# Kernel tuning notes

Hardware: AMD Instinct MI355X
Metric: run time of the kernel (lower is better)

## Reference

```python
import jax, jax.numpy as jnp
import numpy as np

B, N, DIM, H = 8, 1024, 512, 8
D = DIM // H
SCALE = DIM ** -0.5


def setup_inputs() -> dict:
    key = jax.random.key(0)
    ks = jax.random.split(key, 8)
    s = 0.02
    return {
        "x": jax.random.normal(ks[0], (B, N, DIM), dtype=jnp.float32),
        "mask": jax.random.uniform(ks[1], (1, 1, N, N), dtype=jnp.float32),
        "Wqkv1": jax.random.normal(ks[2], (DIM, 3 * DIM), dtype=jnp.float32) * s,
        "bqkv1": jnp.zeros((3 * DIM,), dtype=jnp.float32),
        "Wqkv2": jax.random.normal(ks[3], (DIM, 3 * DIM), dtype=jnp.float32) * s,
        "bqkv2": jnp.zeros((3 * DIM,), dtype=jnp.float32),
        "Wnn1": jax.random.normal(ks[4], (DIM, DIM), dtype=jnp.float32) * s,
        "bnn1": jnp.zeros((DIM,), dtype=jnp.float32),
    }


def _split_heads(qkv, b, n):
    # qkv: [b, n, 3*dim] -> three [b, h, n, d]
    q, k, v = jnp.split(qkv, 3, axis=-1)
    r = lambda t: t.reshape(b, n, H, D).transpose(0, 2, 1, 3)
    return r(q), r(k), r(v)


def reference(x, mask, Wqkv1, bqkv1, Wqkv2, bqkv2, Wnn1, bnn1):
    b, n, dim = x.shape
    # Stage 1: mask-scaled sigmoid attention (no softmax, no scale)
    q, k, v = _split_heads(x @ Wqkv1 + bqkv1, b, n)
    dots = jax.nn.sigmoid(jnp.einsum('bhid,bhjd->bhij', q, k) * mask)
    out1 = jnp.einsum('bhij,bhjd->bhid', dots, v)
    out1 = out1.transpose(0, 2, 1, 3).reshape(b, n, dim)
    # Stage 2: standard scaled softmax attention on stage-1 output
    q, k, v = _split_heads(out1 @ Wqkv2 + bqkv2, b, n)
    attn = jax.nn.softmax(jnp.einsum('bhid,bhjd->bhij', q, k) * SCALE, axis=-1)
    out = jnp.einsum('bhij,bhjd->bhid', attn, v)
    out = out.transpose(0, 2, 1, 3).reshape(b, n, dim)
    # Output projection (dropout is identity in eval mode)
    return out @ Wnn1 + bnn1
```

## Files before the change

### kernel.cpp

```cpp
#include <hip/hip_runtime.h>
#include <hip/hip_bf16.h>
#include <stdint.h>

constexpr int B_ = 8, N_ = 1024, DIM_ = 512, H_ = 8, D_ = 64;
constexpr int BH_ = B_ * H_;
constexpr int M_  = B_ * N_;
constexpr float SCALE_ = 0.04419417382415922f;
constexpr float LOG2E_ = 1.44269504088896f;
constexpr float QSL2E_ = SCALE_ * LOG2E_;

typedef __bf16 bf16x8 __attribute__((ext_vector_type(8)));
typedef float  f32x4  __attribute__((ext_vector_type(4)));
typedef unsigned short u16;
typedef u16 u16x8 __attribute__((ext_vector_type(8)));
typedef u16 u16x4 __attribute__((ext_vector_type(4)));

static __device__ __forceinline__ u16 f2bf(float f) {
  return __builtin_bit_cast(u16, (__bf16)f);
}
static __device__ __forceinline__ bf16x8 ld8(const u16* p) {
  return __builtin_bit_cast(bf16x8, *reinterpret_cast<const u16x8*>(p));
}
static __device__ __forceinline__ f32x4 mfma16(bf16x8 a, bf16x8 b, f32x4 c) {
  return __builtin_amdgcn_mfma_f32_16x16x32_bf16(a, b, c, 0, 0, 0);
}
static __device__ __forceinline__ void gload_lds16(const u16* g, void* l) {
  __builtin_amdgcn_global_load_lds(
      (const __attribute__((address_space(1))) void*)g,
      (__attribute__((address_space(3))) void*)l, 16, 0, 0);
}
#define LGKM0() asm volatile("s_waitcnt lgkmcnt(0)" ::: "memory")
#define VMW(n)  asm volatile("s_waitcnt vmcnt(" #n ")" ::: "memory")

__global__ void k_prep(const float* __restrict__ x, const float* __restrict__ mask,
                       const float* __restrict__ W1, const float* __restrict__ W2,
                       const float* __restrict__ W3,
                       u16* __restrict__ xb, float* __restrict__ mk,
                       u16* __restrict__ W1t, u16* __restrict__ W2t, u16* __restrict__ W3t)
{
  const int b = blockIdx.x, t = threadIdx.x;
  if (b < 4096) {
    int idx = b * 256 + t;
    float4 v = reinterpret_cast<const float4*>(x)[idx];
    u16x4 o; o[0] = f2bf(v.x); o[1] = f2bf(v.y); o[2] = f2bf(v.z); o[3] = f2bf(v.w);
    reinterpret_cast<u16x4*>(xb)[idx] = o;
  } else if (b < 5120) {
    int idx = (b - 4096) * 256 + t;
    float4 v = reinterpret_cast<const float4*>(mask)[idx];
    v.x *= -LOG2E_; v.y *= -LOG2E_; v.z *= -LOG2E_; v.w *= -LOG2E_;
    reinterpret_cast<float4*>(mk)[idx] = v;
  } else if (b < 8192) {
    int idx = (b - 5120) * 256 + t;
    int c = idx >> 9, k = idx & 511;
    W1t[idx] = f2bf(W1[k * 1536 + c]);
  } else if (b < 11264) {
    int idx = (b - 8192) * 256 + t;
    int c = idx >> 9, k = idx & 511;
    float v = W2[k * 1536 + c];
    if (c < 512) v *= QSL2E_;
    W2t[idx] = f2bf(v);
  } else {
    int idx = (b - 11264) * 256 + t;
    int c = idx >> 9, k = idx & 511;
    W3t[idx] = f2bf(W3[k * 512 + c]);
  }
}

template<int NC, int MODE, bool SQ>
__global__ __launch_bounds__(256) void k_gemm(
    const u16* __restrict__ A, const u16* __restrict__ Wt, const float* __restrict__ bias,
    u16* __restrict__ qo, u16* __restrict__ ko, u16* __restrict__ vto, float* __restrict__ fo)
{
  __shared__ __attribute__((aligned(16))) u16 As[2][128 * 32];
  __shared__ __attribute__((aligned(16))) u16 Bs[2][128 * 32];
  const int wv = threadIdx.x >> 6, ln = threadIdx.x & 63;
  const int lr = ln & 15, lg = ln >> 4;
  const int wr = wv >> 1, wc = wv & 1;
  const int nwg = gridDim.x * gridDim.y;
  const int lin = blockIdx.y * gridDim.x + blockIdx.x;
  const int swz = (lin & 7) * (nwg >> 3) + (lin >> 3);
  const int r0 = (swz & 63) * 128;
  const int c0 = (swz >> 6) * 128;

  auto stage = [&](int bufi, int kk) {
#pragma unroll
    for (int q = 0; q < 2; ++q) {
      int L = (wv * 2 + q) * 1024 + ln * 16;
      int row = L >> 6;
      int col = ((L & 63) ^ (((row >> 1) & 3) << 4)) >> 1;
      gload_lds16(A  + (size_t)(r0 + row) * 512 + kk + col, (char*)As[bufi] + (wv * 2 + q) * 1024);
      gload_lds16(Wt + (size_t)(c0 + row) * 512 + kk + col, (char*)Bs[bufi] + (wv * 2 + q) * 1024);
    }
  };
  auto swzld = [&](const u16* tile, int row, int colb) -> bf16x8 {
    int byte = (row << 6) + (colb ^ (((row >> 1) & 3) << 4));
    return __builtin_bit_cast(bf16x8, *reinterpret_cast<const u16x8*>((const char*)tile + byte));
  };

  f32x4 acc[4][4] = {};
  stage(0, 0);
  int buf = 0;
  for (int kk = 0; kk < 512; kk += 32) {
    __syncthreads();
    if (kk + 32 < 512) stage(buf ^ 1, kk + 32);
    bf16x8 af[4], bfb[4];
#pragma unroll
    for (int m = 0; m < 4; ++m) af[m]  = swzld(As[buf], wr * 64 + m * 16 + lr, lg * 16);
#pragma unroll
    for (int n = 0; n < 4; ++n) bfb[n] = swzld(Bs[buf], wc * 64 + n * 16 + lr, lg * 16);
#pragma unroll
    for (int m = 0; m < 4; ++m)
#pragma unroll
      for (int n = 0; n < 4; ++n)
        acc[m][n] = mfma16(af[m], bfb[n], acc[m][n]);
    buf ^= 1;
  }

#pragma unroll
  for (int m = 0; m < 4; ++m)
#pragma unroll
    for (int n = 0; n < 4; ++n) {
      const int gc  = c0 + wc * 64 + n * 16 + lr;
      const int gr0 = r0 + wr * 64 + m * 16 + lg * 4;
      const float bsc = (SQ && gc < 512) ? QSL2E_ : 1.f;
      const float bv = bias[gc] * bsc;
      if (MODE == 0) {
        const int part = gc >> 9, cc = gc & 511;
        const int hh = cc >> 6, dd = cc & 63;
        const int bb = gr0 >> 10, nn = gr0 & 1023;
        const int bh = bb * H_ + hh;
        if (part == 2) {
          u16x4 w;
#pragma unroll
          for (int r = 0; r < 4; ++r) w[r] = f2bf(acc[m][n][r] + bv);
          *reinterpret_cast<u16x4*>(&vto[((size_t)(bh * D_ + dd)) * N_ + nn]) = w;
        } else {
          u16* dst = (part == 0 ? qo : ko) + ((size_t)(bh * N_ + nn)) * D_ + dd;
#pragma unroll
          for (int r = 0; r < 4; ++r) dst[(size_t)r * D_] = f2bf(acc[m][n][r] + bv);
        }
      } else {
#pragma unroll
        for (int r = 0; r < 4; ++r)
          fo[(size_t)(gr0 + r) * NC + gc] = acc[m][n][r] + bv;
      }
    }
}

template<int STAGE>
__global__ __launch_bounds__(512) void k_attn(
    const u16* __restrict__ Q, const u16* __restrict__ K, const u16* __restrict__ Vt,
    const float* __restrict__ mask, u16* __restrict__ O)
{
  __shared__ __attribute__((aligned(16))) u16 Kb[3][64 * 64];
  __shared__ __attribute__((aligned(16))) u16 Vb[3][64 * 64];
  __shared__ __attribute__((aligned(16))) u16 pbuf[8][16][40];
  const int wv = threadIdx.x >> 6, ln = threadIdx.x & 63;
  const int lr = ln & 15, lg = ln >> 4;
  const int lin = blockIdx.y * gridDim.x + blockIdx.x;
  const int swz = (lin & 7) * 64 + (lin >> 3);
  const int bh = swz >> 3;
  const int i0 = (swz & 7) * 128 + wv * 16;
  const size_t base = (size_t)bh * N_ * D_;

  auto stageKV = [&](int bufi, int jt2) {
    int L = wv * 1024 + ln * 16;
    int row = L >> 7;
    int col = ((L & 127) ^ ((row & 7) << 4)) >> 1;
    gload_lds16(K  + base + (size_t)(jt2 + row) * 64 + col,  (char*)Kb[bufi] + wv * 1024);
    gload_lds16(Vt + base + (size_t)row * 1024 + jt2 + col,  (char*)Vb[bufi] + wv * 1024);
  };
  auto swzld = [&](const u16* tile, int row, int colb) -> bf16x8 {
    int byte = (row << 7) + (colb ^ ((row & 7) << 4));
    return __builtin_bit_cast(bf16x8, *reinterpret_cast<const u16x8*>((const char*)tile + byte));
  };

  bf16x8 aq0 = ld8(Q + base + (size_t)(i0 + lr) * D_ + lg * 8);
  bf16x8 aq1 = ld8(Q + base + (size_t)(i0 + lr) * D_ + 32 + lg * 8);

  f32x4 acco[4] = {};
  float ssum_ln = 0.f;

  float4 mk[4];
  const float* mrow = mask + (size_t)(i0 + lr) * N_;
  auto loadmask = [&](int jt2) {
#pragma unroll
    for (int js = 0; js < 4; ++js)
      mk[js] = *reinterpret_cast<const float4*>(&mrow[jt2 + js * 16 + lg * 4]);
  };
  if (STAGE == 1) loadmask(0);

  stageKV(0, 0);
  stageKV(1, 64);
  constexpr int NT = 16;
  for (int t = 0; t < NT; ++t) {
    LGKM0();
    __builtin_amdgcn_s_barrier();
    if (t + 2 < NT) stageKV((t + 2) % 3, (t + 2) * 64);
    if (STAGE == 1) {
      if (t == 0)       VMW(4);
      else if (t == 1)  VMW(8);
      else if (t < 14)  VMW(12);
      else if (t == 14) VMW(10);
      else              VMW(8);
    } else {
      if (t < 14)       VMW(4);
      else if (t == 14) VMW(2);
      else              VMW(0);
    }
    const int cur = t % 3;
    const u16* Kt = Kb[cur];
    const u16* Vtl = Vb[cur];

    f32x4 s[4];
    __builtin_amdgcn_s_setprio(1);
#pragma unroll
    for (int js = 0; js < 4; ++js) {
      int krow = js * 16 + lr;
      bf16x8 bk0 = swzld(Kt, krow, lg * 16);
      bf16x8 bk1 = swzld(Kt, krow, 64 + lg * 16);
      f32x4 z = {};
      z = mfma16(bk0, aq0, z);
      z = mfma16(bk1, aq1, z);
      s[js] = z;
    }
    __builtin_amdgcn_s_setprio(0);

    float ps = 0.f;
#pragma unroll
    for (int h = 0; h < 2; ++h) {
#pragma unroll
      for (int js2 = 0; js2 < 2; ++js2) {
        const int js = h * 2 + js2;
        u16x4 w;
        if (STAGE == 1) {
#pragma unroll
          for (int r = 0; r < 4; ++r) {
            float mkr = (r == 0) ? mk[js].x : (r == 1) ? mk[js].y : (r == 2) ? mk[js].z : mk[js].w;
            float e = exp2f(s[js][r] * mkr);
            w[r] = f2bf(__builtin_amdgcn_rcpf(1.f + e));
          }
        } else {
#pragma unroll
          for (int r = 0; r < 4; ++r) {
            float p = exp2f(s[js][r]);
            ps += p;
            w[r] = f2bf(p);
          }
        }
        *reinterpret_cast<u16x4*>(&pbuf[wv][lr][js2 * 16 + lg * 4]) = w;
      }
      bf16x8 ap = ld8(&pbuf[wv][lr][lg * 8]);
      __builtin_amdgcn_s_setprio(1);
#pragma unroll
      for (int db = 0; db < 4; ++db) {
        bf16x8 bv = swzld(Vtl, db * 16 + lr, h * 64 + lg * 16);
        acco[db] = mfma16(ap, bv, acco[db]);
      }
      __builtin_amdgcn_s_setprio(0);
    }
    if (STAGE == 2) ssum_ln += ps;
    if (STAGE == 1 && t + 1 < NT) loadmask((t + 1) * 64);
  }

  float inv[4];
  if (STAGE == 2) {
    float st = ssum_ln;
    st += __shfl_xor(st, 16);
    st += __shfl_xor(st, 32);
#pragma unroll
    for (int r = 0; r < 4; ++r)
      inv[r] = __builtin_amdgcn_rcpf(__shfl(st, lg * 4 + r));
  }

  const int bb = bh >> 3, hh = bh & 7;
  u16* orow = O + (size_t)(bb * N_ + i0 + lr) * DIM_ + hh * D_;
#pragma unroll
  for (int h = 0; h < 2; ++h) {
#pragma unroll
    for (int db = 0; db < 2; ++db)
#pragma unroll
      for (int r = 0; r < 4; ++r) {
        float v = acco[h * 2 + db][r];
        if (STAGE == 2) v *= inv[r];
        pbuf[wv][lg * 4 + r][db * 16 + lr] = f2bf(v);
      }
    bf16x8 ov = ld8(&pbuf[wv][lr][lg * 8]);
    *reinterpret_cast<u16x8*>(orow + h * 32 + lg * 8) = __builtin_bit_cast(u16x8, ov);
  }
}

extern "C" void kernel_launch(void* const* d_in, const int* in_sizes, int n_in,
                              void* d_out, int out_size, void* d_ws, size_t ws_size,
                              hipStream_t stream)
{
  const float* x    = (const float*)d_in[0];
  const float* mask = (const float*)d_in[1];
  const float* W1   = (const float*)d_in[2];
  const float* b1   = (const float*)d_in[3];
  const float* W2   = (const float*)d_in[4];
  const float* b2   = (const float*)d_in[5];
  const float* W3   = (const float*)d_in[6];
  const float* b3   = (const float*)d_in[7];
  float* out = (float*)d_out;

  char* ws = (char*)d_ws;
  size_t off = 0;
  auto alloc = [&](size_t bytes) { char* p = ws + off; off += (bytes + 255) & ~255ULL; return p; };
  u16*   W1t = (u16*)alloc((size_t)1536 * 512 * 2);
  u16*   W2t = (u16*)alloc((size_t)1536 * 512 * 2);
  u16*   W3t = (u16*)alloc((size_t)512 * 512 * 2);
  u16*   xb  = (u16*)alloc((size_t)M_ * DIM_ * 2);
  u16*   q   = (u16*)alloc((size_t)BH_ * N_ * D_ * 2);
  u16*   k   = (u16*)alloc((size_t)BH_ * N_ * D_ * 2);
  u16*   vt  = (u16*)alloc((size_t)BH_ * N_ * D_ * 2);
  u16*   o1  = (u16*)alloc((size_t)M_ * DIM_ * 2);
  float* mk  = (float*)alloc((size_t)N_ * N_ * 4);
  u16*   o2  = xb;

  k_prep<<<12288, 256, 0, stream>>>(x, mask, W1, W2, W3, xb, mk, W1t, W2t, W3t);

  dim3 g1(M_ / 128, 1536 / 128);
  k_gemm<1536, 0, false><<<g1, 256, 0, stream>>>(xb, W1t, b1, q, k, vt, nullptr);

  dim3 ga(N_ / 128, BH_);
  k_attn<1><<<ga, 512, 0, stream>>>(q, k, vt, mk, o1);

  k_gemm<1536, 0, true><<<g1, 256, 0, stream>>>(o1, W2t, b2, q, k, vt, nullptr);

  k_attn<2><<<ga, 512, 0, stream>>>(q, k, vt, mk, o2);

  dim3 g3(M_ / 128, 512 / 128);
  k_gemm<512, 1, false><<<g3, 256, 0, stream>>>(o2, W3t, b3, nullptr, nullptr, nullptr, out);
}
```

Before: 227.1 us.

## Shrink attention blocks to 4 waves with double-buffered K/V and precomputed LDS offsets

The attention kernel now uses 256-thread blocks covering 64 query rows instead of 512-thread blocks covering 128, with a matching grid and block-index swizzle. The triple-buffered K/V ring with hand-tuned vmcnt waits becomes a double buffer guarded by __syncthreads, and the swizzled LDS read addresses are precomputed once. The aim is to raise occupancy and cut per-iteration address arithmetic. The cost is that K/V tiles are loaded twice as often across blocks, and the prefetch distance drops from two tiles to one.

```diff
diff --git a/kernel.cpp b/kernel.cpp
--- a/kernel.cpp
+++ b/kernel.cpp
@@ -21,6 +21,9 @@
 static __device__ __forceinline__ bf16x8 ld8(const u16* p) {
   return __builtin_bit_cast(bf16x8, *reinterpret_cast<const u16x8*>(p));
 }
+static __device__ __forceinline__ bf16x8 ld8b(const char* p) {
+  return __builtin_bit_cast(bf16x8, *reinterpret_cast<const u16x8*>(p));
+}
 static __device__ __forceinline__ f32x4 mfma16(bf16x8 a, bf16x8 b, f32x4 c) {
   return __builtin_amdgcn_mfma_f32_16x16x32_bf16(a, b, c, 0, 0, 0);
 }
@@ -29,8 +32,6 @@
       (const __attribute__((address_space(1))) void*)g,
       (__attribute__((address_space(3))) void*)l, 16, 0, 0);
 }
-#define LGKM0() asm volatile("s_waitcnt lgkmcnt(0)" ::: "memory")
-#define VMW(n)  asm volatile("s_waitcnt vmcnt(" #n ")" ::: "memory")
 
 __global__ void k_prep(const float* __restrict__ x, const float* __restrict__ mask,
                        const float* __restrict__ W1, const float* __restrict__ W2,
@@ -148,32 +149,40 @@
 }
 
 template<int STAGE>
-__global__ __launch_bounds__(512) void k_attn(
+__global__ __launch_bounds__(256, 4) void k_attn(
     const u16* __restrict__ Q, const u16* __restrict__ K, const u16* __restrict__ Vt,
     const float* __restrict__ mask, u16* __restrict__ O)
 {
-  __shared__ __attribute__((aligned(16))) u16 Kb[3][64 * 64];
-  __shared__ __attribute__((aligned(16))) u16 Vb[3][64 * 64];
-  __shared__ __attribute__((aligned(16))) u16 pbuf[8][16][40];
+  __shared__ __attribute__((aligned(16))) u16 Kb[2][64 * 64];
+  __shared__ __attribute__((aligned(16))) u16 Vb[2][64 * 64];
+  __shared__ __attribute__((aligned(16))) u16 pbuf[4][16][40];
   const int wv = threadIdx.x >> 6, ln = threadIdx.x & 63;
   const int lr = ln & 15, lg = ln >> 4;
   const int lin = blockIdx.y * gridDim.x + blockIdx.x;
-  const int swz = (lin & 7) * 64 + (lin >> 3);
-  const int bh = swz >> 3;
-  const int i0 = (swz & 7) * 128 + wv * 16;
+  const int swz = (lin & 7) * 128 + (lin >> 3);
+  const int bh = swz >> 4;
+  const int i0 = (swz & 15) * 64 + wv * 16;
   const size_t base = (size_t)bh * N_ * D_;
 
-  auto stageKV = [&](int bufi, int jt2) {
-    int L = wv * 1024 + ln * 16;
+  const u16* kp[2]; const u16* vp[2];
+#pragma unroll
+  for (int q = 0; q < 2; ++q) {
+    int L = (wv * 2 + q) * 1024 + ln * 16;
     int row = L >> 7;
     int col = ((L & 127) ^ ((row & 7) << 4)) >> 1;
-    gload_lds16(K  + base + (size_t)(jt2 + row) * 64 + col,  (char*)Kb[bufi] + wv * 1024);
-    gload_lds16(Vt + base + (size_t)row * 1024 + jt2 + col,  (char*)Vb[bufi] + wv * 1024);
+    kp[q] = K  + base + (size_t)row * 64 + col;
+    vp[q] = Vt + base + (size_t)row * 1024 + col;
+  }
+  auto stageKV = [&](int bufi, int jt2) {
+#pragma unroll
+    for (int q = 0; q < 2; ++q) {
+      gload_lds16(kp[q] + (size_t)jt2 * 64, (char*)Kb[bufi] + (wv * 2 + q) * 1024);
+      gload_lds16(vp[q] + jt2,              (char*)Vb[bufi] + (wv * 2 + q) * 1024);
+    }
   };
-  auto swzld = [&](const u16* tile, int row, int colb) -> bf16x8 {
-    int byte = (row << 7) + (colb ^ ((row & 7) << 4));
-    return __builtin_bit_cast(bf16x8, *reinterpret_cast<const u16x8*>((const char*)tile + byte));
-  };
+  const int s_swz = (lr & 7) << 4;
+  const int b0 = lr * 128 + ((lg * 16) ^ s_swz);
+  const int b1 = lr * 128 + ((64 + lg * 16) ^ s_swz);
 
   bf16x8 aq0 = ld8(Q + base + (size_t)(i0 + lr) * D_ + lg * 8);
   bf16x8 aq1 = ld8(Q + base + (size_t)(i0 + lr) * D_ + 32 + lg * 8);
@@ -191,34 +200,19 @@
   if (STAGE == 1) loadmask(0);
 
   stageKV(0, 0);
-  stageKV(1, 64);
-  constexpr int NT = 16;
-  for (int t = 0; t < NT; ++t) {
-    LGKM0();
-    __builtin_amdgcn_s_barrier();
-    if (t + 2 < NT) stageKV((t + 2) % 3, (t + 2) * 64);
-    if (STAGE == 1) {
-      if (t == 0)       VMW(4);
-      else if (t == 1)  VMW(8);
-      else if (t < 14)  VMW(12);
-      else if (t == 14) VMW(10);
-      else              VMW(8);
-    } else {
-      if (t < 14)       VMW(4);
-      else if (t == 14) VMW(2);
-      else              VMW(0);
-    }
-    const int cur = t % 3;
-    const u16* Kt = Kb[cur];
-    const u16* Vtl = Vb[cur];
+  int buf = 0;
+  for (int jt = 0; jt < N_; jt += 64) {
+    __syncthreads();
+    if (jt + 64 < N_) stageKV(buf ^ 1, jt + 64);
+    const char* Kt  = (const char*)Kb[buf];
+    const char* Vtl = (const char*)Vb[buf];
 
     f32x4 s[4];
     __builtin_amdgcn_s_setprio(1);
 #pragma unroll
     for (int js = 0; js < 4; ++js) {
-      int krow = js * 16 + lr;
-      bf16x8 bk0 = swzld(Kt, krow, lg * 16);
-      bf16x8 bk1 = swzld(Kt, krow, 64 + lg * 16);
+      bf16x8 bk0 = ld8b(Kt + b0 + js * 2048);
+      bf16x8 bk1 = ld8b(Kt + b1 + js * 2048);
       f32x4 z = {};
       z = mfma16(bk0, aq0, z);
       z = mfma16(bk1, aq1, z);
@@ -251,16 +245,18 @@
         *reinterpret_cast<u16x4*>(&pbuf[wv][lr][js2 * 16 + lg * 4]) = w;
       }
       bf16x8 ap = ld8(&pbuf[wv][lr][lg * 8]);
+      const int bh_base = (h == 0) ? b0 : b1;
       __builtin_amdgcn_s_setprio(1);
 #pragma unroll
       for (int db = 0; db < 4; ++db) {
-        bf16x8 bv = swzld(Vtl, db * 16 + lr, h * 64 + lg * 16);
+        bf16x8 bv = ld8b(Vtl + bh_base + db * 2048);
         acco[db] = mfma16(ap, bv, acco[db]);
       }
       __builtin_amdgcn_s_setprio(0);
     }
     if (STAGE == 2) ssum_ln += ps;
-    if (STAGE == 1 && t + 1 < NT) loadmask((t + 1) * 64);
+    if (STAGE == 1 && jt + 64 < N_) loadmask(jt + 64);
+    buf ^= 1;
   }
 
   float inv[4];
@@ -323,12 +319,12 @@
   dim3 g1(M_ / 128, 1536 / 128);
   k_gemm<1536, 0, false><<<g1, 256, 0, stream>>>(xb, W1t, b1, q, k, vt, nullptr);
 
-  dim3 ga(N_ / 128, BH_);
-  k_attn<1><<<ga, 512, 0, stream>>>(q, k, vt, mk, o1);
+  dim3 ga(16, BH_);
+  k_attn<1><<<ga, 256, 0, stream>>>(q, k, vt, mk, o1);
 
   k_gemm<1536, 0, true><<<g1, 256, 0, stream>>>(o1, W2t, b2, q, k, vt, nullptr);
 
-  k_attn<2><<<ga, 512, 0, stream>>>(q, k, vt, mk, o2);
+  k_attn<2><<<ga, 256, 0, stream>>>(q, k, vt, mk, o2);
 
   dim3 g3(M_ / 128, 512 / 128);
   k_gemm<512, 1, false><<<g3, 256, 0, stream>>>(o2, W3t, b3, nullptr, nullptr, nullptr, out);
```

Result: slower. 233.1 us (+2.6%).
